# Kernel optimization log

Measured on AMD Instinct MI355X. Metric: run time of the kernel, lower is better.

Reference implementation:

```python
import jax, jax.numpy as jnp
import numpy as np
from jax import lax

CONF_THRES = 0.25
IOU_THRES = 0.45
MAX_WH = 4096.0   # class offset, agnostic=False
MAX_DET = 300
NEG = jnp.float32(-1e30)


def setup_inputs() -> dict:
    key = jax.random.key(0)
    B, N, C = 16, 25200, 85  # 640x640 yolov5, nc=80
    k1, k2, k3, k4 = jax.random.split(key, 4)
    xy = jax.random.uniform(k1, (B, N, 2), jnp.float32, 0.0, 640.0)
    wh = jax.random.uniform(k2, (B, N, 2), jnp.float32, 4.0, 120.0)
    obj = jax.random.uniform(k3, (B, N, 1), jnp.float32)
    cls = jax.random.uniform(k4, (B, N, C - 5), jnp.float32)
    prediction = jnp.concatenate([xy, wh, obj, cls], axis=-1)
    return {"prediction": prediction}


def _xywh2xyxy(b):
    # b: [N,4] (cx,cy,w,h) -> (x1,y1,x2,y2)
    return jnp.concatenate([b[:, :2] - b[:, 2:4] * 0.5,
                            b[:, :2] + b[:, 2:4] * 0.5], axis=1)


def _iou_one_vs_all(box, boxes):
    # box: [4], boxes: [N,4], plain IoU as in torchvision.ops.nms
    x1 = jnp.maximum(box[0], boxes[:, 0])
    y1 = jnp.maximum(box[1], boxes[:, 1])
    x2 = jnp.minimum(box[2], boxes[:, 2])
    y2 = jnp.minimum(box[3], boxes[:, 3])
    inter = jnp.clip(x2 - x1, 0.0) * jnp.clip(y2 - y1, 0.0)
    a1 = (box[2] - box[0]) * (box[3] - box[1])
    a2 = (boxes[:, 2] - boxes[:, 0]) * (boxes[:, 3] - boxes[:, 1])
    return inter / (a1 + a2 - inter)


def _nms_image(p):
    # p: [N, 5+nc] single-image predictions (decoded xywh, obj, class scores)
    obj = p[:, 4]                               # [N]
    cls_scores = p[:, 5:] * obj[:, None]        # x[:,5:] *= x[:,4:5]
    conf = jnp.max(cls_scores, axis=1)          # best-class conf
    j = jnp.argmax(cls_scores, axis=1)          # best class id
    boxes = _xywh2xyxy(p[:, :4])                # [N,4]
    valid = (obj > CONF_THRES) & (conf > CONF_THRES)
    # class-offset boxes for per-class NMS (agnostic=False)
    nms_boxes = boxes + (j.astype(boxes.dtype) * MAX_WH)[:, None]

    s0 = jnp.where(valid, conf, NEG)

    def step(s_live, _):
        i = jnp.argmax(s_live)
        sel = s_live[i]
        keep = sel > 0.0
        iou = _iou_one_vs_all(nms_boxes[i], nms_boxes)
        suppress = keep & (iou > IOU_THRES)
        s_new = jnp.where(suppress, NEG, s_live).at[i].set(NEG)
        return s_new, (i, keep)

    _, (idxs, keeps) = lax.scan(step, s0, None, length=MAX_DET)
    # output rows [x1,y1,x2,y2,conf,cls] — boxes WITHOUT class offset
    rows = jnp.concatenate([boxes[idxs], conf[idxs, None],
                            j[idxs, None].astype(boxes.dtype)], axis=1)
    rows = rows * keeps[:, None].astype(rows.dtype)  # zero padded slots
    return rows, keeps


def reference(prediction):
    # prediction: [B, N, 5+nc] -> ([B, MAX_DET, 6], [B, MAX_DET] keep mask)
    out, keep = jax.vmap(_nms_image)(prediction)
    return out, keep
```

## Files before the change

kernel.cpp:

```cpp
#include <hip/hip_runtime.h>
#include <cstdint>
#include <cfloat>

#define BATCH 16
#define NBOX 25200
#define CH 85
#define NCLS 80
#define CAP 512
#define ACC 48
#define MAXDET 300
#define RPB 128
#define CNTPAD 16

typedef unsigned long long u64;

__device__ __forceinline__ u64 shflx64(u64 v, int m) {
    int lo = __shfl_xor((int)(unsigned)(v & 0xffffffffu), m);
    int hi = __shfl_xor((int)(unsigned)(v >> 32), m);
    return ((u64)(unsigned)hi << 32) | (u64)(unsigned)lo;
}

__global__ __launch_bounds__(256) void pre_kernel(const float* __restrict__ p,
                                                  int* __restrict__ cnt,
                                                  u64* __restrict__ bucketKey) {
#pragma clang fp contract(off)
    __shared__ float s[RPB * CH];
    int tid = threadIdx.x;
    long blockRow = (long)blockIdx.x * RPB;

    const float4* p4 = (const float4*)(p + blockRow * CH);
    float4* s4 = (float4*)s;
    for (int t = tid; t < RPB * CH / 4; t += 256) {
        __builtin_amdgcn_global_load_lds(
            (const __attribute__((address_space(1))) void*)(p4 + t),
            (__attribute__((address_space(3))) void*)(s4 + (t & ~63)),
            16, 0, 0);
    }
    __syncthreads();

    int r = tid >> 1;
    int half = tid & 1;
    const float* row = s + r * CH;
    float obj = row[4];

    float v = -FLT_MAX; int c = 1000;
    int c0 = half * 40;
    for (int k = 0; k < 40; k++) {
        float sc = row[5 + c0 + k] * obj;
        int cc = c0 + k;
        if (sc > v) { v = sc; c = cc; }
    }
    float v2 = __shfl_xor(v, 1);
    int   cz = __shfl_xor(c, 1);
    if (v2 > v || (v2 == v && cz < c)) { v = v2; c = cz; }

    if (half == 0 && obj > 0.25f && v > 0.25f) {
        int wid = (int)blockRow + r;
        int b   = wid / NBOX;
        int idx = wid - b * NBOX;
        u64 key = ((u64)__float_as_uint(v) << 22) | ((u64)(32767 - idx) << 7) | (u64)c;
        int bkt = b * NCLS + c;
        int pos = atomicAdd(&cnt[bkt * CNTPAD], 1);
        if (pos < CAP) bucketKey[(long)bkt * CAP + pos] = key;
    }
}

__global__ __launch_bounds__(256) void nms_kernel(const float* __restrict__ p,
                                                  const int* __restrict__ cnt,
                                                  const u64* __restrict__ bucketKey,
                                                  u64* __restrict__ accKey) {
#pragma clang fp contract(off)
    int lane = threadIdx.x & 63;
    int bkt = (blockIdx.x << 2) | (threadIdx.x >> 6);
    int b = bkt / NCLS, c = bkt - b * NCLS;
    int n = cnt[bkt * CNTPAD]; if (n > CAP) n = CAP;

    u64 key[8];
#pragma unroll
    for (int r = 0; r < 8; r++) {
        int pos = (r << 6) | lane;
        key[r] = (pos < n) ? bucketKey[(long)bkt * CAP + pos] : 0ULL;
    }

    auto CE_lane = [&](int k, int j) {
#pragma unroll
        for (int r = 0; r < 8; r++) {
            u64 part = shflx64(key[r], j);
            int pos = (r << 6) | lane;
            bool keepmax = (((pos & k) == 0) == ((lane & j) == 0));
            u64 mx = (key[r] > part) ? key[r] : part;
            u64 mn = (key[r] > part) ? part : key[r];
            key[r] = keepmax ? mx : mn;
        }
    };

#pragma unroll
    for (int k = 2; k <= 64; k <<= 1)
        for (int j = k >> 1; j > 0; j >>= 1)
            CE_lane(k, j);

#define CE_REG(K, M)                                                   \
    {                                                                  \
        _Pragma("unroll")                                              \
        for (int r = 0; r < 8; r++) if (!(r & (M))) {                  \
            int r2 = r | (M);                                          \
            u64 a = key[r], d = key[r2];                               \
            bool desc = (((r << 6) & (K)) == 0);                       \
            u64 hi = (a > d) ? a : d, lo = (a > d) ? d : a;            \
            key[r]  = desc ? hi : lo;                                  \
            key[r2] = desc ? lo : hi;                                  \
        }                                                              \
    }

    CE_REG(128, 1)
    for (int j = 32; j > 0; j >>= 1) CE_lane(128, j);
    CE_REG(256, 2) CE_REG(256, 1)
    for (int j = 32; j > 0; j >>= 1) CE_lane(256, j);
    CE_REG(512, 4) CE_REG(512, 2) CE_REG(512, 1)
    for (int j = 32; j > 0; j >>= 1) CE_lane(512, j);
#undef CE_REG

    float off = (float)c * 4096.0f;
    float rx1[8], ry1[8], rx2[8], ry2[8], rar[8];
    int live = 0;
#pragma unroll
    for (int r = 0; r < 8; r++) {
        int pos = (r << 6) | lane;
        rx1[r] = 0.f; ry1[r] = 0.f; rx2[r] = 0.f; ry2[r] = 0.f; rar[r] = 0.f;
        if (pos < n) {
            int idx = 32767 - (int)((key[r] >> 7) & 32767);
            const float* q = p + ((long)b * NBOX + idx) * CH;
            float x = q[0], y = q[1], w = q[2], h = q[3];
            float hw = w * 0.5f, hh = h * 0.5f;
            rx1[r] = (x - hw) + off; ry1[r] = (y - hh) + off;
            rx2[r] = (x + hw) + off; ry2[r] = (y + hh) + off;
            rar[r] = (rx2[r] - rx1[r]) * (ry2[r] - ry1[r]);
            live |= 1 << r;
        }
    }

    long obase = (long)bkt * ACC;
    int nacc = 0;
    for (;;) {
        int i = -1;
#pragma unroll
        for (int r = 0; r < 8; r++) {
            u64 mr = __ballot((live >> r) & 1);
            if (i < 0 && mr) i = (r << 6) + (int)__ffsll((long long)mr) - 1;
        }
        if (i < 0) break;
        int ro = i >> 6, owner = i & 63;

        u64 kk; float sX1, sY1, sX2, sY2, sA;
        switch (ro) {
            case 0: kk=key[0]; sX1=rx1[0]; sY1=ry1[0]; sX2=rx2[0]; sY2=ry2[0]; sA=rar[0]; break;
            case 1: kk=key[1]; sX1=rx1[1]; sY1=ry1[1]; sX2=rx2[1]; sY2=ry2[1]; sA=rar[1]; break;
            case 2: kk=key[2]; sX1=rx1[2]; sY1=ry1[2]; sX2=rx2[2]; sY2=ry2[2]; sA=rar[2]; break;
            case 3: kk=key[3]; sX1=rx1[3]; sY1=ry1[3]; sX2=rx2[3]; sY2=ry2[3]; sA=rar[3]; break;
            case 4: kk=key[4]; sX1=rx1[4]; sY1=ry1[4]; sX2=rx2[4]; sY2=ry2[4]; sA=rar[4]; break;
            case 5: kk=key[5]; sX1=rx1[5]; sY1=ry1[5]; sX2=rx2[5]; sY2=ry2[5]; sA=rar[5]; break;
            case 6: kk=key[6]; sX1=rx1[6]; sY1=ry1[6]; sX2=rx2[6]; sY2=ry2[6]; sA=rar[6]; break;
            default:kk=key[7]; sX1=rx1[7]; sY1=ry1[7]; sX2=rx2[7]; sY2=ry2[7]; sA=rar[7]; break;
        }
        if (lane == owner) {
            accKey[obase + nacc] = kk;
            live &= ~(1 << ro);
        }
        nacc++;
        if (nacc == ACC) break;

        float X1 = __shfl(sX1, owner), Y1 = __shfl(sY1, owner);
        float X2 = __shfl(sX2, owner), Y2 = __shfl(sY2, owner);
        float A  = __shfl(sA,  owner);

#pragma unroll
        for (int r = 0; r < 8; r++) {
            if ((live >> r) & 1) {
                float xx1 = fmaxf(X1, rx1[r]);
                float yy1 = fmaxf(Y1, ry1[r]);
                float xx2 = fminf(X2, rx2[r]);
                float yy2 = fminf(Y2, ry2[r]);
                float inter = fmaxf(xx2 - xx1, 0.0f) * fmaxf(yy2 - yy1, 0.0f);
                float uni = (A + rar[r]) - inter;
                if (inter / uni > 0.45f) live &= ~(1 << r);
            }
        }
    }
    for (int t = nacc + lane; t < ACC; t += 64) accKey[obase + t] = 0ULL;
}

__global__ __launch_bounds__(256) void merge_kernel(const float* __restrict__ p,
                                                    const u64* __restrict__ accKey,
                                                    float* __restrict__ outRows,
                                                    float* __restrict__ outKeep) {
#pragma clang fp contract(off)
    __shared__ u64 L[NCLS * ACC];
    int tid = threadIdx.x;
    int b = blockIdx.y;
    const u64* src = accKey + (long)b * NCLS * ACC;
    for (int t = tid; t < NCLS * ACC; t += 256) L[t] = src[t];
    __syncthreads();

    int g = blockIdx.x * 256 + tid;
    u64 key = L[g];
    if (key == 0ULL) return;
    int cOwn = g / ACC;
    int rank = g - cOwn * ACC;

    for (int d = 1; d < NCLS; d++) {
        int c2 = cOwn + d; if (c2 >= NCLS) c2 -= NCLS;
        const u64* Lc = L + c2 * ACC;
        int cn = 0;
#pragma unroll
        for (int s2 = 32; s2; s2 >>= 1) {
            int nc = cn + s2;
            if (nc <= ACC && Lc[nc - 1] > key) cn = nc;
        }
        rank += cn;
        if (rank >= MAXDET) return;
    }

    int cc  = (int)(key & 127);
    int idx = 32767 - (int)((key >> 7) & 32767);
    float conf = __uint_as_float((unsigned)(key >> 22));
    const float* q = p + ((long)b * NBOX + idx) * CH;
    float x = q[0], y = q[1], w = q[2], h = q[3];
    float hw = w * 0.5f, hh = h * 0.5f;
    float* row = outRows + ((long)b * MAXDET + rank) * 6;
    row[0] = x - hw; row[1] = y - hh; row[2] = x + hw; row[3] = y + hh;
    row[4] = conf;   row[5] = (float)cc;
    outKeep[b * MAXDET + rank] = 1.0f;
}

extern "C" void kernel_launch(void* const* d_in, const int* in_sizes, int n_in,
                              void* d_out, int out_size, void* d_ws, size_t ws_size,
                              hipStream_t stream) {
    const float* p = (const float*)d_in[0];
    float* out = (float*)d_out;

    char* ws = (char*)d_ws;
    int* cnt = (int*)ws;
    u64* bucketKey = (u64*)(ws + BATCH * NCLS * CNTPAD * 4);
    u64* accKey    = (u64*)(ws + BATCH * NCLS * CNTPAD * 4
                               + (size_t)BATCH * NCLS * CAP * 8);

    hipMemsetAsync(cnt, 0, BATCH * NCLS * CNTPAD * sizeof(int), stream);
    hipMemsetAsync(out, 0, (size_t)out_size * sizeof(float), stream);
    pre_kernel<<<(BATCH * NBOX) / RPB, 256, 0, stream>>>(p, cnt, bucketKey);
    nms_kernel<<<BATCH * NCLS / 4, 256, 0, stream>>>(p, cnt, bucketKey, accKey);
    dim3 gM(NCLS * ACC / 256, BATCH);
    merge_kernel<<<gM, 256, 0, stream>>>(p, accKey, out, out + (size_t)BATCH * MAXDET * 6);
}
```

Baseline: 308.2 us.

## Segment bucket counters, fold output memset into pre-kernel, unroll merge rank search

```diff
diff --git a/kernel.cpp b/kernel.cpp
--- a/kernel.cpp
+++ b/kernel.cpp
@@ -7,9 +7,10 @@
 #define CH 85
 #define NCLS 80
 #define CAP 512
+#define SEGCAP 128
 #define ACC 48
 #define MAXDET 300
-#define RPB 128
+#define RPB 112
 #define CNTPAD 16
 
 typedef unsigned long long u64;
@@ -22,10 +23,16 @@
 
 __global__ __launch_bounds__(256) void pre_kernel(const float* __restrict__ p,
                                                   int* __restrict__ cnt,
-                                                  u64* __restrict__ bucketKey) {
+                                                  u64* __restrict__ bucketKey,
+                                                  float* __restrict__ outZero,
+                                                  int outN) {
 #pragma clang fp contract(off)
     __shared__ float s[RPB * CH];
     int tid = threadIdx.x;
+
+    long z = (long)blockIdx.x * 256 + tid;
+    if (z < outN) outZero[z] = 0.0f;
+
     long blockRow = (long)blockIdx.x * RPB;
 
     const float4* p4 = (const float4*)(p + blockRow * CH);
@@ -40,28 +47,31 @@
 
     int r = tid >> 1;
     int half = tid & 1;
-    const float* row = s + r * CH;
-    float obj = row[4];
-
-    float v = -FLT_MAX; int c = 1000;
-    int c0 = half * 40;
-    for (int k = 0; k < 40; k++) {
-        float sc = row[5 + c0 + k] * obj;
-        int cc = c0 + k;
-        if (sc > v) { v = sc; c = cc; }
-    }
-    float v2 = __shfl_xor(v, 1);
-    int   cz = __shfl_xor(c, 1);
-    if (v2 > v || (v2 == v && cz < c)) { v = v2; c = cz; }
-
-    if (half == 0 && obj > 0.25f && v > 0.25f) {
-        int wid = (int)blockRow + r;
-        int b   = wid / NBOX;
-        int idx = wid - b * NBOX;
-        u64 key = ((u64)__float_as_uint(v) << 22) | ((u64)(32767 - idx) << 7) | (u64)c;
-        int bkt = b * NCLS + c;
-        int pos = atomicAdd(&cnt[bkt * CNTPAD], 1);
-        if (pos < CAP) bucketKey[(long)bkt * CAP + pos] = key;
+    if (r < RPB) {
+        const float* row = s + r * CH;
+        float obj = row[4];
+
+        float v = -FLT_MAX; int c = 1000;
+        int c0 = half * 40;
+        for (int k = 0; k < 40; k++) {
+            float sc = row[5 + c0 + k] * obj;
+            int cc = c0 + k;
+            if (sc > v) { v = sc; c = cc; }
+        }
+        float v2 = __shfl_xor(v, 1);
+        int   cz = __shfl_xor(c, 1);
+        if (v2 > v || (v2 == v && cz < c)) { v = v2; c = cz; }
+
+        if (half == 0 && obj > 0.25f && v > 0.25f) {
+            int wid = (int)blockRow + r;
+            int b   = wid / NBOX;
+            int idx = wid - b * NBOX;
+            u64 key = ((u64)__float_as_uint(v) << 22) | ((u64)(32767 - idx) << 7) | (u64)c;
+            int bkt = b * NCLS + c;
+            int seg = idx & 3;
+            int pos = atomicAdd(&cnt[bkt * CNTPAD + seg], 1);
+            if (pos < SEGCAP) bucketKey[(long)bkt * CAP + seg * SEGCAP + pos] = key;
+        }
     }
 }
 
@@ -73,13 +83,21 @@
     int lane = threadIdx.x & 63;
     int bkt = (blockIdx.x << 2) | (threadIdx.x >> 6);
     int b = bkt / NCLS, c = bkt - b * NCLS;
-    int n = cnt[bkt * CNTPAD]; if (n > CAP) n = CAP;
+
+    const int* cb = cnt + bkt * CNTPAD;
+    int ns[4];
+#pragma unroll
+    for (int s2 = 0; s2 < 4; s2++) {
+        int v = cb[s2];
+        ns[s2] = (v < SEGCAP) ? v : SEGCAP;
+    }
+    int ntot = ns[0] + ns[1] + ns[2] + ns[3];
 
     u64 key[8];
 #pragma unroll
     for (int r = 0; r < 8; r++) {
-        int pos = (r << 6) | lane;
-        key[r] = (pos < n) ? bucketKey[(long)bkt * CAP + pos] : 0ULL;
+        int off = ((r & 1) << 6) | lane;
+        key[r] = (off < ns[r >> 1]) ? bucketKey[(long)bkt * CAP + (r << 6) + lane] : 0ULL;
     }
 
     auto CE_lane = [&](int k, int j) {
@@ -127,7 +145,7 @@
     for (int r = 0; r < 8; r++) {
         int pos = (r << 6) | lane;
         rx1[r] = 0.f; ry1[r] = 0.f; rx2[r] = 0.f; ry2[r] = 0.f; rar[r] = 0.f;
-        if (pos < n) {
+        if (pos < ntot) {
             int idx = 32767 - (int)((key[r] >> 7) & 32767);
             const float* q = p + ((long)b * NBOX + idx) * CH;
             float x = q[0], y = q[1], w = q[2], h = q[3];
@@ -145,8 +163,10 @@
         int i = -1;
 #pragma unroll
         for (int r = 0; r < 8; r++) {
-            u64 mr = __ballot((live >> r) & 1);
-            if (i < 0 && mr) i = (r << 6) + (int)__ffsll((long long)mr) - 1;
+            if (i < 0) {
+                u64 mr = __ballot((live >> r) & 1);
+                if (mr) i = (r << 6) + (int)__ffsll((long long)mr) - 1;
+            }
         }
         if (i < 0) break;
         int ro = i >> 6, owner = i & 63;
@@ -169,9 +189,11 @@
         nacc++;
         if (nacc == ACC) break;
 
-        float X1 = __shfl(sX1, owner), Y1 = __shfl(sY1, owner);
-        float X2 = __shfl(sX2, owner), Y2 = __shfl(sY2, owner);
-        float A  = __shfl(sA,  owner);
+        float X1 = __int_as_float(__builtin_amdgcn_readlane(__float_as_int(sX1), owner));
+        float Y1 = __int_as_float(__builtin_amdgcn_readlane(__float_as_int(sY1), owner));
+        float X2 = __int_as_float(__builtin_amdgcn_readlane(__float_as_int(sX2), owner));
+        float Y2 = __int_as_float(__builtin_amdgcn_readlane(__float_as_int(sY2), owner));
+        float A  = __int_as_float(__builtin_amdgcn_readlane(__float_as_int(sA),  owner));
 
 #pragma unroll
         for (int r = 0; r < 8; r++) {
@@ -207,14 +229,36 @@
     int cOwn = g / ACC;
     int rank = g - cOwn * ACC;
 
-    for (int d = 1; d < NCLS; d++) {
+    int d = 1;
+    for (; d + 3 < NCLS; d += 4) {
+        int ca = cOwn + d;     if (ca >= NCLS) ca -= NCLS;
+        int cb = cOwn + d + 1; if (cb >= NCLS) cb -= NCLS;
+        int cc = cOwn + d + 2; if (cc >= NCLS) cc -= NCLS;
+        int cd = cOwn + d + 3; if (cd >= NCLS) cd -= NCLS;
+        const u64* LA = L + ca * ACC;
+        const u64* LB = L + cb * ACC;
+        const u64* LC = L + cc * ACC;
+        const u64* LD = L + cd * ACC;
+        int na = 0, nb = 0, nc = 0, nd = 0;
+#pragma unroll
+        for (int s2 = 32; s2; s2 >>= 1) {
+            int ta = na + s2, tb = nb + s2, tc = nc + s2, td = nd + s2;
+            if (ta <= ACC && LA[ta - 1] > key) na = ta;
+            if (tb <= ACC && LB[tb - 1] > key) nb = tb;
+            if (tc <= ACC && LC[tc - 1] > key) nc = tc;
+            if (td <= ACC && LD[td - 1] > key) nd = td;
+        }
+        rank += na + nb + nc + nd;
+        if (rank >= MAXDET) return;
+    }
+    for (; d < NCLS; d++) {
         int c2 = cOwn + d; if (c2 >= NCLS) c2 -= NCLS;
         const u64* Lc = L + c2 * ACC;
         int cn = 0;
 #pragma unroll
         for (int s2 = 32; s2; s2 >>= 1) {
-            int nc = cn + s2;
-            if (nc <= ACC && Lc[nc - 1] > key) cn = nc;
+            int ncx = cn + s2;
+            if (ncx <= ACC && Lc[ncx - 1] > key) cn = ncx;
         }
         rank += cn;
         if (rank >= MAXDET) return;
@@ -245,8 +289,7 @@
                                + (size_t)BATCH * NCLS * CAP * 8);
 
     hipMemsetAsync(cnt, 0, BATCH * NCLS * CNTPAD * sizeof(int), stream);
-    hipMemsetAsync(out, 0, (size_t)out_size * sizeof(float), stream);
-    pre_kernel<<<(BATCH * NBOX) / RPB, 256, 0, stream>>>(p, cnt, bucketKey);
+    pre_kernel<<<(BATCH * NBOX) / RPB, 256, 0, stream>>>(p, cnt, bucketKey, out, out_size);
     nms_kernel<<<BATCH * NCLS / 4, 256, 0, stream>>>(p, cnt, bucketKey, accKey);
     dim3 gM(NCLS * ACC / 256, BATCH);
     merge_kernel<<<gM, 256, 0, stream>>>(p, accKey, out, out + (size_t)BATCH * MAXDET * 6);
```

New measurement: 288.4 us. 1.07x faster.
